# Optimization experiments

Measured on AMD Instinct MI355X. Metric: run time of the kernel, lower is better.

## Reference

```python
import jax, jax.numpy as jnp
import numpy as np

B, V, S, H = 16384, 16, 64, 512


def setup_inputs() -> dict:
    key = jax.random.key(0)
    kx, kw, kb, kws, kbs = jax.random.split(key, 5)
    x = jax.random.normal(kx, (B, V, S), dtype=jnp.float32)
    # per-variable linear layers: weight [V, S, H], bias [V, H]
    W = jax.random.normal(kw, (V, S, H), dtype=jnp.float32) * (1.0 / np.sqrt(S))
    b = jax.random.normal(kb, (V, H), dtype=jnp.float32) * 0.01
    # variable selection linear: hidden -> V
    W_sel = jax.random.normal(kws, (H, V), dtype=jnp.float32) * (1.0 / np.sqrt(H))
    b_sel = jax.random.normal(kbs, (V,), dtype=jnp.float32) * 0.01
    return {"x": x, "W": W, "b": b, "W_sel": W_sel, "b_sel": b_sel}


def reference(x, W, b, W_sel, b_sel):
    # per-variable linears: [B, V, H]
    transformed = jnp.einsum('bvs,vsh->bvh', x, W) + b  # grouped small GEMMs
    # torch stacks to [B, H, V]; mean over variable axis -> [B, H]
    flat = transformed.mean(axis=1)
    # softmax-gated selection weights [B, V] (dropout is identity in eval)
    weights = jax.nn.softmax(flat @ W_sel + b_sel, axis=-1)
    # weighted sum over variables -> [B, H]
    out = jnp.einsum('bvh,bv->bh', transformed, weights)
    return out
```

## Files before the change

### kernel.cpp

```cpp
#include <hip/hip_runtime.h>
#include <hip/hip_bf16.h>
#include <stdint.h>

#define B_ROWS 16384
#define VDIM   16
#define SDIM   64
#define HDIM   512
#define KDIM   1024
#define KP2    1088
#define BK     64

#define ASTR     1064
#define G_PLOG   68096
#define G_WLDS   (68096 + 8704)
#define G_LDS    (68096 + 8704 + 2048)

using bf16x8 = __attribute__((ext_vector_type(8))) __bf16;
using u16x8  = __attribute__((ext_vector_type(8))) unsigned short;
using f32x4  = __attribute__((ext_vector_type(4))) float;

__device__ __forceinline__ unsigned short f2bf(float f) {
  unsigned int u = __builtin_bit_cast(unsigned int, f);
  u = (u + 0x7FFFu + ((u >> 16) & 1u)) >> 16;
  return (unsigned short)u;
}
__device__ __forceinline__ float bf2f(unsigned short s) {
  return __builtin_bit_cast(float, (unsigned int)s << 16);
}

__device__ __forceinline__ void gl_lds16(const void* g, void* l) {
  __builtin_amdgcn_global_load_lds(
      (const __attribute__((address_space(1))) unsigned int*)(uintptr_t)g,
      (__attribute__((address_space(3))) unsigned int*)(unsigned int)(uintptr_t)l,
      16, 0, 0);
}

__global__ __launch_bounds__(256) void k0_prep(
    const float* __restrict__ W, const float* __restrict__ bias,
    const float* __restrict__ Wsel, const float* __restrict__ bsel,
    unsigned short* __restrict__ Bt, unsigned short* __restrict__ WcombT,
    float* __restrict__ bcomb) {
  __shared__ float bm[HDIM];
  __shared__ float part[16][17];
  __shared__ unsigned short tile[32][264];
  const int t = threadIdx.x;
  if (blockIdx.x < 68) {
    const int k0 = (blockIdx.x >> 1) * 32;
    const int n  = ((blockIdx.x & 1) << 8) + t;
    #pragma unroll 8
    for (int kk = 0; kk < 32; ++kk) {
      const int k = k0 + kk;
      float val;
      if (k < KDIM)            val = W[(size_t)k * HDIM + n];
      else if (k < KDIM + 16)  val = bias[(size_t)(k - KDIM) * HDIM + n];
      else                     val = 0.f;
      tile[kk][t] = f2bf(val);
    }
    __syncthreads();
    unsigned short* dst = Bt + (size_t)n * KP2 + k0;
    #pragma unroll
    for (int seg = 0; seg < 4; ++seg) {
      unsigned short o[8];
      #pragma unroll
      for (int jj = 0; jj < 8; ++jj) o[jj] = tile[seg * 8 + jj][t];
      *(u16x8*)(dst + seg * 8) = *(const u16x8*)o;
    }
    return;
  }
  const int bid = blockIdx.x - 68;
  if (bid < 256) {
    const int wave = t >> 6, lane = t & 63;
    const int k = bid * 4 + wave;
    const float* wr = W + (size_t)k * HDIM;
    float s[16];
    #pragma unroll
    for (int v = 0; v < 16; ++v) s[v] = 0.f;
    #pragma unroll
    for (int j = 0; j < 8; ++j) {
      const int h = lane + 64 * j;
      const float a = wr[h];
      const float4* wl = (const float4*)(Wsel + h * 16);
      const float4 q0 = wl[0], q1 = wl[1], q2 = wl[2], q3 = wl[3];
      s[0]  = fmaf(a, q0.x, s[0]);  s[1]  = fmaf(a, q0.y, s[1]);
      s[2]  = fmaf(a, q0.z, s[2]);  s[3]  = fmaf(a, q0.w, s[3]);
      s[4]  = fmaf(a, q1.x, s[4]);  s[5]  = fmaf(a, q1.y, s[5]);
      s[6]  = fmaf(a, q1.z, s[6]);  s[7]  = fmaf(a, q1.w, s[7]);
      s[8]  = fmaf(a, q2.x, s[8]);  s[9]  = fmaf(a, q2.y, s[9]);
      s[10] = fmaf(a, q2.z, s[10]); s[11] = fmaf(a, q2.w, s[11]);
      s[12] = fmaf(a, q3.x, s[12]); s[13] = fmaf(a, q3.y, s[13]);
      s[14] = fmaf(a, q3.z, s[14]); s[15] = fmaf(a, q3.w, s[15]);
    }
    #pragma unroll
    for (int off = 32; off > 0; off >>= 1) {
      #pragma unroll
      for (int v = 0; v < 16; ++v) s[v] += __shfl_xor(s[v], off, 64);
    }
    float mine = 0.f;
    #pragma unroll
    for (int v = 0; v < 16; ++v) mine = (lane == v) ? s[v] : mine;
    if (lane < 16) WcombT[lane * KDIM + k] = f2bf(mine * (1.f / 16.f));
  } else {
    for (int h = t; h < HDIM; h += 256) {
      float s = 0.f;
      #pragma unroll
      for (int v = 0; v < VDIM; ++v) s += bias[v * HDIM + h];
      bm[h] = s * (1.f / 16.f);
    }
    __syncthreads();
    int v = t & 15, sl = t >> 4;
    float s = 0.f;
    for (int h = sl * 32; h < sl * 32 + 32; ++h) s = fmaf(bm[h], Wsel[h * VDIM + v], s);
    part[sl][v] = s;
    __syncthreads();
    if (t < 16) {
      float s2 = bsel[t];
      #pragma unroll
      for (int i = 0; i < 16; ++i) s2 += part[i][t];
      bcomb[t] = s2;
    }
  }
}

__global__ __launch_bounds__(512, 4) void k1_gate(
    const float* __restrict__ x, const unsigned short* __restrict__ WcombT,
    const float* __restrict__ bcomb, unsigned short* __restrict__ Ap,
    int rowbase) {
  extern __shared__ unsigned short As[];
  float* plog = (float*)((char*)As + G_PLOG);
  float* wlds = (float*)((char*)As + G_WLDS);

  const int t = threadIdx.x;
  const int lrow0 = blockIdx.x * 32;
  const int grow0 = rowbase + lrow0;
  const int wave = t >> 6, lane = t & 63;
  const int mlane = lane & 15, quad = lane >> 4;
  const int srow = t >> 4;
  const int sc = (t & 15) * 8;

  u16x8 xreg[8];
  {
    const float* xr = x + (size_t)(grow0 + srow) * KDIM + sc;
    unsigned short* aw = As + srow * ASTR + sc;
    #pragma unroll
    for (int i = 0; i < 8; ++i) {
      const f32x4 a0 = __builtin_nontemporal_load((const f32x4*)(xr + i * 128));
      const f32x4 a1 = __builtin_nontemporal_load((const f32x4*)(xr + i * 128 + 4));
      u16x8 u;
      u[0] = f2bf(a0[0]); u[1] = f2bf(a0[1]); u[2] = f2bf(a0[2]); u[3] = f2bf(a0[3]);
      u[4] = f2bf(a1[0]); u[5] = f2bf(a1[1]); u[6] = f2bf(a1[2]); u[7] = f2bf(a1[3]);
      xreg[i] = u;
      *(u16x8*)(aw + i * 128) = u;
    }
  }
  __syncthreads();

  {
    const int kh = wave >> 1, rg = wave & 1;
    const unsigned short* al = As + (rg * 16 + mlane) * ASTR + kh * 256 + quad * 8;
    const unsigned short* bl = WcombT + mlane * KDIM + kh * 256 + quad * 8;
    f32x4 acc = {0.f, 0.f, 0.f, 0.f};
    #pragma unroll
    for (int kt = 0; kt < 8; ++kt) {
      bf16x8 a = *(const bf16x8*)al; al += 32;
      bf16x8 b = *(const bf16x8*)bl; bl += 32;
      acc = __builtin_amdgcn_mfma_f32_16x16x32_bf16(a, b, acc, 0, 0, 0);
    }
    float* pl = plog + ((size_t)((kh * 2 + rg) * 16 + quad * 4) * 17 + mlane);
    #pragma unroll
    for (int r = 0; r < 4; ++r) pl[r * 17] = acc[r];
  }
  __syncthreads();

  if (t < 32) {
    const int rg = t >> 4, rr = t & 15;
    float l[16];
    float mx = -1e30f;
    #pragma unroll
    for (int v = 0; v < 16; ++v) {
      float s = bcomb[v];
      #pragma unroll
      for (int kq = 0; kq < 4; ++kq)
        s += plog[((size_t)((kq * 2 + rg) * 16 + rr)) * 17 + v];
      l[v] = s;
      mx = fmaxf(mx, s);
    }
    float s = 0.f;
    #pragma unroll
    for (int v = 0; v < 16; ++v) { l[v] = __expf(l[v] - mx); s += l[v]; }
    const float inv = 1.f / s;
    float* wo = wlds + t * 16;
    #pragma unroll
    for (int v = 0; v < 16; ++v) wo[v] = l[v] * inv;
  }
  __syncthreads();

  {
    float wv[16];
    const f32x4* wq = (const f32x4*)(wlds + srow * 16);
    #pragma unroll
    for (int q = 0; q < 4; ++q) {
      const f32x4 f = wq[q];
      wv[4 * q + 0] = f[0]; wv[4 * q + 1] = f[1];
      wv[4 * q + 2] = f[2]; wv[4 * q + 3] = f[3];
    }
    const int vbase = (t & 15) >> 3;
    unsigned short* aw = Ap + (size_t)(lrow0 + srow) * KP2 + sc;
    #pragma unroll
    for (int i = 0; i < 8; ++i) {
      const float w = wv[2 * i + vbase];
      const u16x8 a = xreg[i];
      u16x8 o;
      #pragma unroll
      for (int j = 0; j < 8; ++j) o[j] = f2bf(w * bf2f(a[j]));
      *(u16x8*)(aw + i * 128) = o;
    }
    const int seg = t & 15;
    if (seg < 8) {
      u16x8 o;
      #pragma unroll
      for (int jj = 0; jj < 8; ++jj) {
        const int c = seg * 8 + jj;
        o[jj] = (c < 16) ? f2bf(wv[c]) : (unsigned short)0;
      }
      *(u16x8*)(Ap + (size_t)(lrow0 + srow) * KP2 + KDIM + seg * 8) = o;
    }
  }
}

__global__ __launch_bounds__(256) void k2_gemm(
    const unsigned short* __restrict__ Ap, const unsigned short* __restrict__ Bt,
    float* __restrict__ C, int rowbase) {
  __shared__ unsigned short As[2][128 * BK];
  __shared__ unsigned short Bs[2][128 * BK];

  const int t = threadIdx.x;
  const int nwg = gridDim.x;
  const int q = nwg >> 3, r = nwg & 7;
  const int xcd = blockIdx.x & 7, idx = blockIdx.x >> 3;
  const int bid = (xcd < r ? xcd * (q + 1) : r * (q + 1) + (xcd - r) * q) + idx;

  const int lrowb = (bid >> 2) * 128;
  const int colb  = (bid & 3) * 128;
  const int wave = t >> 6, lane = t & 63;
  const int mlane = lane & 15, quad = lane >> 4;
  const int wr = wave >> 1, wc = wave & 1;

  const int l8 = lane >> 3, lk = (lane & 7) * 8;
  const unsigned short* asrc[4];
  const unsigned short* bsrc[4];
  #pragma unroll
  for (int i = 0; i < 4; ++i) {
    asrc[i] = Ap + (size_t)(lrowb + wave * 32 + i * 8 + l8) * KP2 + lk;
    bsrc[i] = Bt + (size_t)(colb + wave * 32 + i * 8 + l8) * KP2 + lk;
  }
  const int ldst = (wave * 32) * BK;

  #pragma unroll
  for (int i = 0; i < 4; ++i) gl_lds16(asrc[i], &As[0][ldst + i * 8 * BK]);
  #pragma unroll
  for (int i = 0; i < 4; ++i) gl_lds16(bsrc[i], &Bs[0][ldst + i * 8 * BK]);
  #pragma unroll
  for (int i = 0; i < 4; ++i) { asrc[i] += BK; bsrc[i] += BK; }
  asm volatile("s_waitcnt vmcnt(0)" ::: "memory");
  __builtin_amdgcn_s_barrier();
  __builtin_amdgcn_sched_barrier(0);

  f32x4 acc[4][4];
  const f32x4 z = {0.f, 0.f, 0.f, 0.f};
  #pragma unroll
  for (int i = 0; i < 4; ++i)
    #pragma unroll
    for (int j = 0; j < 4; ++j) acc[i][j] = z;

  #pragma unroll 1
  for (int kt = 0; kt < 17; ++kt) {
    const int cur = kt & 1;
    if (kt < 16) {
      #pragma unroll
      for (int i = 0; i < 4; ++i) gl_lds16(asrc[i], &As[cur ^ 1][ldst + i * 8 * BK]);
      #pragma unroll
      for (int i = 0; i < 4; ++i) gl_lds16(bsrc[i], &Bs[cur ^ 1][ldst + i * 8 * BK]);
      #pragma unroll
      for (int i = 0; i < 4; ++i) { asrc[i] += BK; bsrc[i] += BK; }
    }
    #pragma unroll
    for (int ks = 0; ks < 2; ++ks) {
      bf16x8 av[4], bv[4];
      #pragma unroll
      for (int i = 0; i < 4; ++i)
        av[i] = *(const bf16x8*)(&As[cur][(wr * 64 + i * 16 + mlane) * BK + ks * 32 + quad * 8]);
      #pragma unroll
      for (int j = 0; j < 4; ++j)
        bv[j] = *(const bf16x8*)(&Bs[cur][(wc * 64 + j * 16 + mlane) * BK + ks * 32 + quad * 8]);
      #pragma unroll
      for (int i = 0; i < 4; ++i)
        #pragma unroll
        for (int j = 0; j < 4; ++j)
          acc[i][j] = __builtin_amdgcn_mfma_f32_16x16x32_bf16(av[i], bv[j], acc[i][j], 0, 0, 0);
    }
    __builtin_amdgcn_sched_barrier(0);
    asm volatile("s_waitcnt vmcnt(0)" ::: "memory");
    __builtin_amdgcn_s_barrier();
    __builtin_amdgcn_sched_barrier(0);
  }

  #pragma unroll
  for (int i = 0; i < 4; ++i)
    #pragma unroll
    for (int j = 0; j < 4; ++j)
      #pragma unroll
      for (int r2 = 0; r2 < 4; ++r2) {
        const size_t row = (size_t)rowbase + lrowb + wr * 64 + i * 16 + quad * 4 + r2;
        const int col = colb + wc * 64 + j * 16 + mlane;
        __builtin_nontemporal_store(acc[i][j][r2], &C[row * HDIM + col]);
      }
}

extern "C" void kernel_launch(void* const* d_in, const int* in_sizes, int n_in,
                              void* d_out, int out_size, void* d_ws, size_t ws_size,
                              hipStream_t stream) {
  const float* x    = (const float*)d_in[0];
  const float* W    = (const float*)d_in[1];
  const float* bias = (const float*)d_in[2];
  const float* Wsel = (const float*)d_in[3];
  const float* bsel = (const float*)d_in[4];
  float* out = (float*)d_out;

  char* ws = (char*)d_ws;
  unsigned short* Bt     = (unsigned short*)(ws);
  unsigned short* WcombT = (unsigned short*)(ws + 1114112);
  float*          bcomb  = (float*)(ws + 1146880);
  unsigned short* Ap     = (unsigned short*)(ws + 1147136);

  const size_t fixed = 1147136;
  size_t avail = (ws_size > fixed) ? (ws_size - fixed) : 0;
  size_t maxRows = avail / (KP2 * 2);
  int sliceRows = (int)((maxRows / 128) * 128);
  if (sliceRows > B_ROWS) sliceRows = B_ROWS;
  if (sliceRows < 128) sliceRows = 128;

  static int lds_set = 0;
  if (!lds_set) {
    hipFuncSetAttribute((const void*)k1_gate,
                        hipFuncAttributeMaxDynamicSharedMemorySize, G_LDS);
    lds_set = 1;
  }

  k0_prep<<<325, 256, 0, stream>>>(W, bias, Wsel, bsel, Bt, WcombT, bcomb);
  for (int r0 = 0; r0 < B_ROWS; r0 += sliceRows) {
    const int rows = (B_ROWS - r0 < sliceRows) ? (B_ROWS - r0) : sliceRows;
    k1_gate<<<rows / 32, 512, G_LDS, stream>>>(x, WcombT, bcomb, Ap, r0);
    k2_gemm<<<(rows / 128) * 4, 256, 0, stream>>>(Ap, Bt, out, r0);
  }
}
```

Measured before the change: 161.6 us.

## Load GEMM B operand directly into registers, drop its LDS staging

```diff
diff --git a/kernel.cpp b/kernel.cpp
--- a/kernel.cpp
+++ b/kernel.cpp
@@ -227,11 +227,10 @@
   }
 }
 
-__global__ __launch_bounds__(256) void k2_gemm(
+__global__ __launch_bounds__(256, 3) void k2_gemm(
     const unsigned short* __restrict__ Ap, const unsigned short* __restrict__ Bt,
     float* __restrict__ C, int rowbase) {
   __shared__ unsigned short As[2][128 * BK];
-  __shared__ unsigned short Bs[2][128 * BK];
 
   const int t = threadIdx.x;
   const int nwg = gridDim.x;
@@ -247,20 +246,28 @@
 
   const int l8 = lane >> 3, lk = (lane & 7) * 8;
   const unsigned short* asrc[4];
+  #pragma unroll
+  for (int i = 0; i < 4; ++i)
+    asrc[i] = Ap + (size_t)(lrowb + wave * 32 + i * 8 + l8) * KP2 + lk;
+  const int ldst = (wave * 32) * BK;
+
   const unsigned short* bsrc[4];
   #pragma unroll
-  for (int i = 0; i < 4; ++i) {
-    asrc[i] = Ap + (size_t)(lrowb + wave * 32 + i * 8 + l8) * KP2 + lk;
-    bsrc[i] = Bt + (size_t)(colb + wave * 32 + i * 8 + l8) * KP2 + lk;
-  }
-  const int ldst = (wave * 32) * BK;
+  for (int j = 0; j < 4; ++j)
+    bsrc[j] = Bt + (size_t)(colb + wc * 64 + j * 16 + mlane) * KP2 + quad * 8;
 
   #pragma unroll
   for (int i = 0; i < 4; ++i) gl_lds16(asrc[i], &As[0][ldst + i * 8 * BK]);
   #pragma unroll
-  for (int i = 0; i < 4; ++i) gl_lds16(bsrc[i], &Bs[0][ldst + i * 8 * BK]);
-  #pragma unroll
-  for (int i = 0; i < 4; ++i) { asrc[i] += BK; bsrc[i] += BK; }
+  for (int i = 0; i < 4; ++i) asrc[i] += BK;
+  bf16x8 bcur[2][4], bnext[2][4];
+  #pragma unroll
+  for (int ks = 0; ks < 2; ++ks)
+    #pragma unroll
+    for (int j = 0; j < 4; ++j)
+      bcur[ks][j] = *(const bf16x8*)(bsrc[j] + ks * 32);
+  #pragma unroll
+  for (int j = 0; j < 4; ++j) bsrc[j] += BK;
   asm volatile("s_waitcnt vmcnt(0)" ::: "memory");
   __builtin_amdgcn_s_barrier();
   __builtin_amdgcn_sched_barrier(0);
@@ -279,25 +286,31 @@
       #pragma unroll
       for (int i = 0; i < 4; ++i) gl_lds16(asrc[i], &As[cur ^ 1][ldst + i * 8 * BK]);
       #pragma unroll
-      for (int i = 0; i < 4; ++i) gl_lds16(bsrc[i], &Bs[cur ^ 1][ldst + i * 8 * BK]);
-      #pragma unroll
-      for (int i = 0; i < 4; ++i) { asrc[i] += BK; bsrc[i] += BK; }
+      for (int i = 0; i < 4; ++i) asrc[i] += BK;
+      #pragma unroll
+      for (int ks = 0; ks < 2; ++ks)
+        #pragma unroll
+        for (int j = 0; j < 4; ++j)
+          bnext[ks][j] = *(const bf16x8*)(bsrc[j] + ks * 32);
+      #pragma unroll
+      for (int j = 0; j < 4; ++j) bsrc[j] += BK;
     }
     #pragma unroll
     for (int ks = 0; ks < 2; ++ks) {
-      bf16x8 av[4], bv[4];
+      bf16x8 av[4];
       #pragma unroll
       for (int i = 0; i < 4; ++i)
         av[i] = *(const bf16x8*)(&As[cur][(wr * 64 + i * 16 + mlane) * BK + ks * 32 + quad * 8]);
-      #pragma unroll
-      for (int j = 0; j < 4; ++j)
-        bv[j] = *(const bf16x8*)(&Bs[cur][(wc * 64 + j * 16 + mlane) * BK + ks * 32 + quad * 8]);
       #pragma unroll
       for (int i = 0; i < 4; ++i)
         #pragma unroll
         for (int j = 0; j < 4; ++j)
-          acc[i][j] = __builtin_amdgcn_mfma_f32_16x16x32_bf16(av[i], bv[j], acc[i][j], 0, 0, 0);
-    }
+          acc[i][j] = __builtin_amdgcn_mfma_f32_16x16x32_bf16(av[i], bcur[ks][j], acc[i][j], 0, 0, 0);
+    }
+    #pragma unroll
+    for (int ks = 0; ks < 2; ++ks)
+      #pragma unroll
+      for (int j = 0; j < 4; ++j) bcur[ks][j] = bnext[ks][j];
     __builtin_amdgcn_sched_barrier(0);
     asm volatile("s_waitcnt vmcnt(0)" ::: "memory");
     __builtin_amdgcn_s_barrier();
```

New measurement: 175.0 us. +8.3%, slower.
